# Optimization experiments

Hardware: AMD Instinct MI355X
Metric: run time of the kernel (lower is better)

The kernel has to match this reference:

```python
import jax, jax.numpy as jnp
import numpy as np

WS = 8          # window_size
SHIFT = 4       # shift_size
HEADS = 12
C = 384
HD = C // HEADS
SCALE = HD ** -0.5
N = WS * WS


def _rel_pos_index(Wh, Ww):
    # double_step_seq(2*Ww-1, Wh, 1, Ww) -> (1, Wh*Ww); idx = rel + rel.T; flip along axis 1
    seq1 = np.arange(0, (2 * Ww - 1) * Wh, 2 * Ww - 1)
    seq2 = np.arange(0, Ww)
    rel = (seq1[:, None] + seq2[None, :]).reshape(1, -1)
    idx = rel + rel.T
    return np.flip(idx, 1).copy()

REL_IDX = jnp.asarray(_rel_pos_index(WS, WS))  # [N, N] int


def window_partition(x, ws):
    # x: [B, H, W, C] -> [B*nW, ws*ws, C]
    B, H, W, Cc = x.shape
    x = x.reshape(B, H // ws, ws, W // ws, ws, Cc).transpose(0, 1, 3, 2, 4, 5)
    return x.reshape(-1, ws * ws, Cc)


def window_reverse(win, H, W, ws):
    B = win.shape[0] // ((H // ws) * (W // ws))
    x = win.reshape(B, H // ws, W // ws, ws, ws, -1).transpose(0, 1, 3, 2, 4, 5)
    return x.reshape(B, H, W, -1)


def _attn_mask(H, W, ws, shift):
    # region ids 0..8 per (h,w) as in the torch slice loop
    hi = np.arange(H)
    wi = np.arange(W)
    h_id = (hi >= H - ws).astype(np.int32) + (hi >= H - shift).astype(np.int32)
    w_id = (wi >= W - ws).astype(np.int32) + (wi >= W - shift).astype(np.int32)
    cnt = (h_id[:, None] * 3 + w_id[None, :]).astype(np.float32)
    img = jnp.asarray(cnt)[None, :, :, None]              # [1, H, W, 1]
    mw = window_partition(img, ws).reshape(-1, ws * ws)   # [nW, N]
    diff = mw[:, None, :] - mw[:, :, None]                # [nW, N, N]
    return jnp.where(diff != 0, jnp.float32(-100.0), jnp.float32(0.0))


def setup_inputs() -> dict:
    key = jax.random.key(0)
    ks = jax.random.split(key, 8)
    B, H, W = 16, 96, 96
    std = 0.02
    return {
        "query": jax.random.normal(ks[0], (B, H * W, C), jnp.float32),
        "skip_query": jax.random.normal(ks[1], (B, H * W, C), jnp.float32),
        "W_qkv": jax.random.normal(ks[2], (C, 2 * C), jnp.float32) * std,
        "b_qkv": jnp.zeros((2 * C,), jnp.float32),
        "W_skip": jax.random.normal(ks[3], (C, C), jnp.float32) * std,
        "b_skip": jnp.zeros((C,), jnp.float32),
        "rpb_table": jax.random.normal(ks[4], ((2 * WS - 1) * (2 * WS - 1), HEADS), jnp.float32) * std,
        "W_proj": jax.random.normal(ks[5], (C, C), jnp.float32) * std,
        "b_proj": jnp.zeros((C,), jnp.float32),
        "h": H,
        "w": W,
    }


def reference(query, skip_query, W_qkv, b_qkv, W_skip, b_skip, rpb_table, W_proj, b_proj, h, w):
    B, L, Cc = query.shape
    q4 = query.reshape(B, h, w, Cc)
    s4 = skip_query.reshape(B, h, w, Cc)
    pad_r = (WS - w % WS) % WS
    pad_b = (WS - h % WS) % WS
    q4 = jnp.pad(q4, ((0, 0), (0, pad_b), (0, pad_r), (0, 0)))
    s4 = jnp.pad(s4, ((0, 0), (0, pad_b), (0, pad_r), (0, 0)))
    H_pad, W_pad = q4.shape[1], q4.shape[2]

    # cyclic shift
    q4 = jnp.roll(q4, (-SHIFT, -SHIFT), axis=(1, 2))
    s4 = jnp.roll(s4, (-SHIFT, -SHIFT), axis=(1, 2))
    mask = _attn_mask(H_pad, W_pad, WS, SHIFT)  # [nW, N, N]

    xw = window_partition(q4, WS)   # [Bn, N, C] -> k, v source
    sw = window_partition(s4, WS)   # [Bn, N, C] -> q source
    Bn = xw.shape[0]

    kv = (xw @ W_qkv + b_qkv).reshape(Bn, N, 2, HEADS, HD)
    k = kv[:, :, 0].transpose(0, 2, 1, 3)   # [Bn, H, N, d]
    v = kv[:, :, 1].transpose(0, 2, 1, 3)
    q = ((sw @ W_skip + b_skip).reshape(Bn, N, HEADS, HD).transpose(0, 2, 1, 3)) * SCALE

    attn = jnp.einsum('bhnd,bhmd->bhnm', q, k)  # [Bn, H, N, N]
    rpb = rpb_table[REL_IDX.reshape(-1)].reshape(N, N, HEADS).transpose(2, 0, 1)
    attn = attn + rpb[None]
    nW = mask.shape[0]
    attn = (attn.reshape(B, nW, HEADS, N, N) + mask[None, :, None]).reshape(Bn, HEADS, N, N)
    attn = jax.nn.softmax(attn, axis=-1)

    out = jnp.einsum('bhnm,bhmd->bhnd', attn, v).transpose(0, 2, 1, 3).reshape(Bn, N, Cc)
    out = out @ W_proj + b_proj

    x4 = window_reverse(out.reshape(-1, WS, WS, Cc), H_pad, W_pad, WS)
    x4 = jnp.roll(x4, (SHIFT, SHIFT), axis=(1, 2))
    x4 = x4[:, :h, :w]
    return x4.reshape(B, h * w, Cc)
```

## Files before the change

### kernel.cpp

```cpp
#include <hip/hip_runtime.h>
#include <hip/hip_bf16.h>


typedef __attribute__((ext_vector_type(8))) short short8;
typedef __attribute__((ext_vector_type(4))) float floatx4;

#define MFMA16(a, b, c) __builtin_amdgcn_mfma_f32_16x16x32_bf16(a, b, c, 0, 0, 0)

__device__ __forceinline__ short f2bf(float f) {
    __hip_bfloat16 h = __float2bfloat16(f);
    return *reinterpret_cast<short*>(&h);
}

__device__ __forceinline__ unsigned cvt2bf(float lo, float hi) {
    unsigned r;
    asm("v_cvt_pk_bf16_f32 %0, %1, %2" : "=v"(r) : "v"(lo), "v"(hi));
    return r;
}

__device__ __forceinline__ void glds16(const void* g, void* l) {
    __builtin_amdgcn_global_load_lds(
        (const __attribute__((address_space(1))) void*)g,
        (__attribute__((address_space(3))) void*)l, 16, 0, 0);
}

__device__ __forceinline__ void lds_fence() {
    asm volatile("s_waitcnt lgkmcnt(0)" ::: "memory");
    __builtin_amdgcn_sched_barrier(0);
}


__global__ __launch_bounds__(256) void prep_wt(const float* __restrict__ Wqkv,
                                               const float* __restrict__ Wskip,
                                               short* __restrict__ Wt) {
    int tid = blockIdx.x * 256 + threadIdx.x;
    if (tid >= 384 * 144) return;
    int k = tid / 144;
    int n8 = (tid % 144) * 8;
#pragma unroll
    for (int e = 0; e < 8; e++) {
        int n = n8 + e;
        float v = (n < 768) ? Wqkv[k * 768 + n]
                            : Wskip[k * 384 + (n - 768)] * 0.17677669529663687f;
        Wt[(size_t)n * 384 + k] = f2bf(v);
    }
}

__global__ __launch_bounds__(256) void prep_wtp(const float* __restrict__ Wproj,
                                                short* __restrict__ WtP) {
    int tid = blockIdx.x * 256 + threadIdx.x;
    if (tid >= 384 * 48) return;
    int k = tid / 48;
    int n8 = (tid % 48) * 8;
#pragma unroll
    for (int e = 0; e < 8; e++) {
        int n = n8 + e;
        WtP[(size_t)n * 384 + k] = f2bf(Wproj[k * 384 + n]);
    }
}

__global__ __launch_bounds__(256) void prep_bias(const float* __restrict__ rpb,
                                                 float* __restrict__ bias64) {
    int tid = blockIdx.x * 256 + threadIdx.x;
    if (tid >= 49152) return;
    int h = tid >> 12;
    int rem = tid & 4095;
    int i = rem >> 6, kk = rem & 63;
    int j = 63 - kk;
    int ridx = 15 * (i >> 3) + (i & 7) + 15 * (j >> 3) + (j & 7);
    bias64[tid] = rpb[ridx * 12 + h];
}

__global__ __launch_bounds__(768, 1) void fused_win(
    const float* __restrict__ xq, const float* __restrict__ xs,
    const short* __restrict__ Wt, const short* __restrict__ WtP,
    const float* __restrict__ bqkv, const float* __restrict__ bskip,
    const float* __restrict__ bproj, const float* __restrict__ bias64,
    float* __restrict__ out) {
    __shared__ short smem[73728];

    const int win = blockIdx.x;
    const int tid = threadIdx.x, lane = tid & 63, wid = tid >> 6;
    const int l15 = lane & 15, g4 = lane >> 4;
    const int al7 = l15 & 7;
    const int brd = (g4 ^ ((l15 ^ (l15 >> 2)) & 3)) * 8;

    const int b_img = win / 144, wr = win % 144;
    const int wy = wr / 12, wx = wr % 12;

    const int gr = tid / 12, gj = tid - gr * 12;
    int gyy = wy * 8 + (gr >> 3) + 4; if (gyy >= 96) gyy -= 96;
    int gxx = wx * 8 + (gr & 7) + 4;  if (gxx >= 96) gxx -= 96;
    const size_t grow = ((size_t)b_img * 9216 + gyy * 96 + gxx) * 384;
    short* lrow = smem + gr * 384;
    const int gr7 = gr & 7;

    auto gatherA = [&](const float* src) {
        const float* rb = src + grow;
#pragma unroll
        for (int cc = 0; cc < 4; cc++) {
            int c = gj * 4 + cc;
            float4 f0 = *(const float4*)(rb + c * 8);
            float4 f1 = *(const float4*)(rb + c * 8 + 4);
            uint4 u;
            u.x = cvt2bf(f0.x, f0.y); u.y = cvt2bf(f0.z, f0.w);
            u.z = cvt2bf(f1.x, f1.y); u.w = cvt2bf(f1.z, f1.w);
            *(uint4*)(lrow + ((c ^ gr7) * 8)) = u;
        }
    };

    const int swst = ((lane >> 2) ^ (lane >> 4)) & 3;
    int bso[2];
#pragma unroll
    for (int j = 0; j < 2; j++)
        bso[j] = (j * 16 + (lane >> 2)) * 384 + (((lane & 3) ^ swst) * 8);
    short* wsc = smem + 24576 + wid * 4096;

    const short* sK = Wt + (size_t)(wid * 32) * 384;
    const short* sV = Wt + (size_t)(384 + wid * 32) * 384;
    const short* sQ = Wt + (size_t)(768 + wid * 32) * 384;
    const short* sP = WtP + (size_t)(wid * 32) * 384;

#pragma unroll
    for (int s = 0; s < 2; s++)
#pragma unroll
        for (int j = 0; j < 2; j++)
            glds16(sQ + bso[j] + s * 32, wsc + s * 1024 + j * 512);
    gatherA(xs);
    __syncthreads();

    floatx4 aq[2][4];
#pragma unroll
    for (int a = 0; a < 2; a++)
#pragma unroll
        for (int b = 0; b < 4; b++)
#pragma unroll
            for (int r = 0; r < 4; r++) aq[a][b][r] = 0.f;
#pragma unroll
    for (int kt = 0; kt < 12; ++kt) {
        if (kt == 11) asm volatile("s_waitcnt vmcnt(0)" ::: "memory");
        else          asm volatile("s_waitcnt vmcnt(2)" ::: "memory");
        const int choff = ((kt * 4 + g4) ^ al7) * 8;
        short* hb = wsc + (kt & 1) * 1024;
        short8 af[4], bq[2];
#pragma unroll
        for (int b = 0; b < 4; b++)
            af[b] = *(const short8*)(smem + (b * 16 + l15) * 384 + choff);
#pragma unroll
        for (int a = 0; a < 2; a++)
            bq[a] = *(const short8*)(hb + (a * 16 + l15) * 32 + brd);
        __builtin_amdgcn_sched_barrier(0);
        asm volatile("s_waitcnt lgkmcnt(0)" ::: "memory");
        if (kt < 10) {
            int ko = (kt + 2) * 32;
#pragma unroll
            for (int j = 0; j < 2; j++) glds16(sQ + bso[j] + ko, hb + j * 512);
        }
        __builtin_amdgcn_sched_barrier(0);
#pragma unroll
        for (int a = 0; a < 2; a++)
#pragma unroll
            for (int b = 0; b < 4; b++)
                aq[a][b] = MFMA16(bq[a], af[b], aq[a][b]);
    }

    const float scl = 0.17677669529663687f;
#pragma unroll
    for (int a = 0; a < 2; a++) {
        float4 bv = *(const float4*)(bskip + wid * 32 + a * 16 + g4 * 4);
#pragma unroll
        for (int b = 0; b < 4; b++) {
            uint2 pk;
            pk.x = cvt2bf(aq[a][b][0] + bv.x * scl, aq[a][b][1] + bv.y * scl);
            pk.y = cvt2bf(aq[a][b][2] + bv.z * scl, aq[a][b][3] + bv.w * scl);
            *(uint2*)(wsc + 1024 + (b * 16 + l15) * 32 + a * 16 + g4 * 4) = pk;
        }
    }
    short8 qf[4];
#pragma unroll
    for (int nj = 0; nj < 4; nj++)
        qf[nj] = *(const short8*)(wsc + 1024 + (nj * 16 + l15) * 32 + g4 * 8);
    lds_fence();

#pragma unroll
    for (int s = 0; s < 2; s++)
#pragma unroll
        for (int j = 0; j < 2; j++) {
            glds16(sK + bso[j] + s * 32, wsc + s * 2048 + j * 512);
            glds16(sV + bso[j] + s * 32, wsc + s * 2048 + 1024 + j * 512);
        }
    __syncthreads();
    gatherA(xq);
    __syncthreads();

    floatx4 ak[2][4], av[2][4];
#pragma unroll
    for (int a = 0; a < 2; a++)
#pragma unroll
        for (int b = 0; b < 4; b++)
#pragma unroll
            for (int r = 0; r < 4; r++) { ak[a][b][r] = 0.f; av[a][b][r] = 0.f; }
#pragma unroll
    for (int kt = 0; kt < 12; ++kt) {
        if (kt == 11) asm volatile("s_waitcnt vmcnt(0)" ::: "memory");
        else          asm volatile("s_waitcnt vmcnt(4)" ::: "memory");
        const int choff = ((kt * 4 + g4) ^ al7) * 8;
        short* hb = wsc + (kt & 1) * 2048;
        short8 af[4], bk[2], bv2[2];
#pragma unroll
        for (int b = 0; b < 4; b++)
            af[b] = *(const short8*)(smem + (b * 16 + l15) * 384 + choff);
#pragma unroll
        for (int a = 0; a < 2; a++) {
            bk[a]  = *(const short8*)(hb + (a * 16 + l15) * 32 + brd);
            bv2[a] = *(const short8*)(hb + 1024 + (a * 16 + l15) * 32 + brd);
        }
        __builtin_amdgcn_sched_barrier(0);
        asm volatile("s_waitcnt lgkmcnt(0)" ::: "memory");
        if (kt < 10) {
            int ko = (kt + 2) * 32;
#pragma unroll
            for (int j = 0; j < 2; j++) {
                glds16(sK + bso[j] + ko, hb + j * 512);
                glds16(sV + bso[j] + ko, hb + 1024 + j * 512);
            }
        }
        __builtin_amdgcn_sched_barrier(0);
#pragma unroll
        for (int a = 0; a < 2; a++)
#pragma unroll
            for (int b = 0; b < 4; b++) {
                ak[a][b] = MFMA16(bk[a], af[b], ak[a][b]);
                av[a][b] = MFMA16(af[b], bv2[a], av[a][b]);
            }
    }
    __syncthreads();

#pragma unroll
    for (int a = 0; a < 2; a++) {
        float4 bv = *(const float4*)(bqkv + wid * 32 + a * 16 + g4 * 4);
#pragma unroll
        for (int b = 0; b < 4; b++) {
            uint2 pk;
            pk.x = cvt2bf(ak[a][b][0] + bv.x, ak[a][b][1] + bv.y);
            pk.y = cvt2bf(ak[a][b][2] + bv.z, ak[a][b][3] + bv.w);
            *(uint2*)(wsc + (b * 16 + l15) * 32 + a * 16 + g4 * 4) = pk;
        }
    }
#pragma unroll
    for (int a = 0; a < 2; a++) {
        float bvs = bqkv[384 + wid * 32 + a * 16 + l15];
#pragma unroll
        for (int b = 0; b < 4; b++) {
            uint2 pk;
            pk.x = cvt2bf(av[a][b][0] + bvs, av[a][b][1] + bvs);
            pk.y = cvt2bf(av[a][b][2] + bvs, av[a][b][3] + bvs);
            int tch = b * 2 + (g4 >> 1);
            *(uint2*)(wsc + 2048 + (a * 16 + l15) * 64 +
                      ((tch ^ (l15 & 7)) * 8) + (g4 & 1) * 4) = pk;
        }
    }
    short8 kf[4], vf[2][2];
#pragma unroll
    for (int mi = 0; mi < 4; mi++)
        kf[mi] = *(const short8*)(wsc + (mi * 16 + l15) * 32 + g4 * 8);
#pragma unroll
    for (int ma = 0; ma < 2; ma++)
#pragma unroll
        for (int ks = 0; ks < 2; ks++)
            vf[ma][ks] = *(const short8*)(wsc + 2048 + (ma * 16 + l15) * 64 +
                                          (((ks * 4 + g4) ^ (l15 & 7)) * 8));

    floatx4 st[4][4];
#pragma unroll
    for (int mi = 0; mi < 4; mi++)
#pragma unroll
        for (int nj = 0; nj < 4; nj++)
#pragma unroll
            for (int r = 0; r < 4; r++) st[mi][nj][r] = 0.f;
#pragma unroll
    for (int mi = 0; mi < 4; mi++)
#pragma unroll
        for (int nj = 0; nj < 4; nj++)
            st[mi][nj] = MFMA16(kf[mi], qf[nj], st[mi][nj]);

    const float* bb = bias64 + wid * 4096;
#pragma unroll
    for (int nj = 0; nj < 4; nj++) {
        int i = nj * 16 + l15;
#pragma unroll
        for (int mi = 0; mi < 4; mi++) {
            floatx4 b4 = *(const floatx4*)(bb + i * 64 + mi * 16 + g4 * 4);
            st[mi][nj] += b4;
        }
    }

    if (wy == 11 || wx == 11) {
        int wy11 = (wy == 11), wx11 = (wx == 11);
        int ri[4];
#pragma unroll
        for (int nj = 0; nj < 4; nj++) {
            int t = nj * 16 + l15;
            int hh = wy11 ? (((t >> 3) >= 4) ? 2 : 1) : 0;
            int ww = wx11 ? (((t & 7) >= 4) ? 2 : 1) : 0;
            ri[nj] = hh * 3 + ww;
        }
#pragma unroll
        for (int mi = 0; mi < 4; mi++)
#pragma unroll
            for (int r = 0; r < 4; r++) {
                int t = mi * 16 + g4 * 4 + r;
                int hh = wy11 ? (((t >> 3) >= 4) ? 2 : 1) : 0;
                int ww = wx11 ? (((t & 7) >= 4) ? 2 : 1) : 0;
                int rk = hh * 3 + ww;
#pragma unroll
                for (int nj = 0; nj < 4; nj++)
                    if (rk != ri[nj]) st[mi][nj][r] -= 100.0f;
            }
    }

    float rden[4];
#pragma unroll
    for (int nj = 0; nj < 4; nj++) {
        float m = -1e30f;
#pragma unroll
        for (int mi = 0; mi < 4; mi++)
#pragma unroll
            for (int r = 0; r < 4; r++) m = fmaxf(m, st[mi][nj][r]);
        m = fmaxf(m, __shfl_xor(m, 16));
        m = fmaxf(m, __shfl_xor(m, 32));
        float s = 0.f;
#pragma unroll
        for (int mi = 0; mi < 4; mi++)
#pragma unroll
            for (int r = 0; r < 4; r++) {
                float p = __expf(st[mi][nj][r] - m);
                st[mi][nj][r] = p;
                s += p;
            }
        s += __shfl_xor(s, 16);
        s += __shfl_xor(s, 32);
        rden[nj] = 1.0f / s;
    }

#pragma unroll
    for (int mi = 0; mi < 4; mi++)
#pragma unroll
        for (int nj = 0; nj < 4; nj++) {
            uint2 pk;
            pk.x = cvt2bf(st[mi][nj][0], st[mi][nj][1]);
            pk.y = cvt2bf(st[mi][nj][2], st[mi][nj][3]);
            int kch = mi * 2 + (g4 >> 1);
            *(uint2*)(wsc + (nj * 16 + l15) * 64 +
                      ((kch ^ (l15 & 7)) * 8) + (g4 & 1) * 4) = pk;
        }

    floatx4 o[2][4];
#pragma unroll
    for (int ma = 0; ma < 2; ma++)
#pragma unroll
        for (int nj = 0; nj < 4; nj++)
#pragma unroll
            for (int r = 0; r < 4; r++) o[ma][nj][r] = 0.f;
#pragma unroll
    for (int ks = 0; ks < 2; ks++) {
        short8 pb[4];
#pragma unroll
        for (int nj = 0; nj < 4; nj++)
            pb[nj] = *(const short8*)(wsc + (nj * 16 + l15) * 64 +
                                      (((ks * 4 + g4) ^ (l15 & 7)) * 8));
#pragma unroll
        for (int ma = 0; ma < 2; ma++)
#pragma unroll
            for (int nj = 0; nj < 4; nj++)
                o[ma][nj] = MFMA16(vf[ma][ks], pb[nj], o[ma][nj]);
    }
    lds_fence();

#pragma unroll
    for (int s = 0; s < 2; s++)
#pragma unroll
        for (int j = 0; j < 2; j++)
            glds16(sP + bso[j] + s * 32, wsc + s * 1024 + j * 512);

#pragma unroll
    for (int ma = 0; ma < 2; ma++)
#pragma unroll
        for (int nj = 0; nj < 4; nj++) {
            int i = nj * 16 + l15;
            uint2 pk;
            pk.x = cvt2bf(o[ma][nj][0] * rden[nj], o[ma][nj][1] * rden[nj]);
            pk.y = cvt2bf(o[ma][nj][2] * rden[nj], o[ma][nj][3] * rden[nj]);
            int ch = wid * 4 + ma * 2 + (g4 >> 1);
            *(uint2*)(smem + i * 384 + ((ch ^ (i & 7)) * 8) + (g4 & 1) * 4) = pk;
        }
    __syncthreads();

    floatx4 ap[2][4];
#pragma unroll
    for (int a = 0; a < 2; a++)
#pragma unroll
        for (int b = 0; b < 4; b++)
#pragma unroll
            for (int r = 0; r < 4; r++) ap[a][b][r] = 0.f;
#pragma unroll
    for (int kt = 0; kt < 12; ++kt) {
        if (kt == 11) asm volatile("s_waitcnt vmcnt(0)" ::: "memory");
        else          asm volatile("s_waitcnt vmcnt(2)" ::: "memory");
        const int choff = ((kt * 4 + g4) ^ al7) * 8;
        short* hb = wsc + (kt & 1) * 1024;
        short8 af[4], bp[2];
#pragma unroll
        for (int b = 0; b < 4; b++)
            af[b] = *(const short8*)(smem + (b * 16 + l15) * 384 + choff);
#pragma unroll
        for (int a = 0; a < 2; a++)
            bp[a] = *(const short8*)(hb + (a * 16 + l15) * 32 + brd);
        __builtin_amdgcn_sched_barrier(0);
        asm volatile("s_waitcnt lgkmcnt(0)" ::: "memory");
        if (kt < 10) {
            int ko = (kt + 2) * 32;
#pragma unroll
            for (int j = 0; j < 2; j++) glds16(sP + bso[j] + ko, hb + j * 512);
        }
        __builtin_amdgcn_sched_barrier(0);
#pragma unroll
        for (int a = 0; a < 2; a++)
#pragma unroll
            for (int b = 0; b < 4; b++)
                ap[a][b] = MFMA16(bp[a], af[b], ap[a][b]);
    }

#pragma unroll
    for (int a = 0; a < 2; a++) {
        int n = wid * 32 + a * 16 + g4 * 4;
        float4 bv = *(const float4*)(bproj + n);
#pragma unroll
        for (int b = 0; b < 4; b++) {
            int t = b * 16 + l15;
            int yy = wy * 8 + (t >> 3) + 4; if (yy >= 96) yy -= 96;
            int xx = wx * 8 + (t & 7) + 4;  if (xx >= 96) xx -= 96;
            floatx4 ov = ap[a][b];
            ov[0] += bv.x; ov[1] += bv.y; ov[2] += bv.z; ov[3] += bv.w;
            *(floatx4*)(&out[((size_t)b_img * 9216 + yy * 96 + xx) * 384 + n]) = ov;
        }
    }
}

extern "C" void kernel_launch(void* const* d_in, const int* in_sizes, int n_in,
                              void* d_out, int out_size, void* d_ws, size_t ws_size,
                              hipStream_t stream) {
    const float* query = (const float*)d_in[0];
    const float* skipq = (const float*)d_in[1];
    const float* Wqkv  = (const float*)d_in[2];
    const float* bqkv  = (const float*)d_in[3];
    const float* Wskip = (const float*)d_in[4];
    const float* bskip = (const float*)d_in[5];
    const float* rpb   = (const float*)d_in[6];
    const float* Wproj = (const float*)d_in[7];
    const float* bproj = (const float*)d_in[8];
    float* out = (float*)d_out;

    int M = in_sizes[0] / 384;
    int nwin = M / 64;

    char* ws = (char*)d_ws;
    size_t off = 0;
    auto alloc = [&](size_t bytes) -> void* {
        void* p = ws + off;
        off = (off + bytes + 255) & ~(size_t)255;
        return p;
    };
    short* Wt     = (short*)alloc((size_t)1152 * 384 * 2);
    short* WtP    = (short*)alloc((size_t)384 * 384 * 2);
    float* bias64 = (float*)alloc((size_t)12 * 64 * 64 * 4);
    (void)ws_size;

    hipLaunchKernelGGL(prep_wt, dim3(216), dim3(256), 0, stream, Wqkv, Wskip, Wt);
    hipLaunchKernelGGL(prep_wtp, dim3(72), dim3(256), 0, stream, Wproj, WtP);
    hipLaunchKernelGGL(prep_bias, dim3(192), dim3(256), 0, stream, rpb, bias64);
    hipLaunchKernelGGL(fused_win, dim3(nwin), dim3(768), 0, stream,
                       query, skipq, Wt, WtP, bqkv, bskip, bproj, bias64, out);
}
```

Before: 498.5 us.

## Prefetch query rows into registers, swizzle Q/K LDS staging, coalesce output stores

The fp32 query rows for the K/V projection are now loaded into registers early, overlapping the Q-projection loop, and converted to bf16 into LDS afterwards instead of running a second gather. The Q and K LDS staging buffers get an XOR swizzle to reduce bank conflicts on their write/read patterns. The output epilogue goes through LDS with a swizzled layout so each wave writes contiguous 128-byte row segments instead of scattered 16-byte stores. In exchange it uses 32 more VGPRs for the prefetched rows, which may hurt occupancy, and adds an extra LDS round trip in the epilogue.

```diff
diff --git a/kernel.cpp b/kernel.cpp
--- a/kernel.cpp
+++ b/kernel.cpp
@@ -127,6 +127,15 @@
         for (int j = 0; j < 2; j++)
             glds16(sQ + bso[j] + s * 32, wsc + s * 1024 + j * 512);
     gatherA(xs);
+    float4 xr[8];
+    {
+        const float* rb = xq + grow;
+#pragma unroll
+        for (int cc = 0; cc < 4; cc++) {
+            xr[cc * 2]     = *(const float4*)(rb + (gj * 4 + cc) * 8);
+            xr[cc * 2 + 1] = *(const float4*)(rb + (gj * 4 + cc) * 8 + 4);
+        }
+    }
     __syncthreads();
 
     floatx4 aq[2][4];
@@ -173,13 +182,17 @@
             uint2 pk;
             pk.x = cvt2bf(aq[a][b][0] + bv.x * scl, aq[a][b][1] + bv.y * scl);
             pk.y = cvt2bf(aq[a][b][2] + bv.z * scl, aq[a][b][3] + bv.w * scl);
-            *(uint2*)(wsc + 1024 + (b * 16 + l15) * 32 + a * 16 + g4 * 4) = pk;
+            int row = b * 16 + l15;
+            int phys = (a * 2 + (g4 >> 1)) ^ (row & 3);
+            *(uint2*)(wsc + 1024 + row * 32 + phys * 8 + (g4 & 1) * 4) = pk;
         }
     }
     short8 qf[4];
 #pragma unroll
-    for (int nj = 0; nj < 4; nj++)
-        qf[nj] = *(const short8*)(wsc + 1024 + (nj * 16 + l15) * 32 + g4 * 8);
+    for (int nj = 0; nj < 4; nj++) {
+        int row = nj * 16 + l15;
+        qf[nj] = *(const short8*)(wsc + 1024 + row * 32 + ((g4 ^ (row & 3)) * 8));
+    }
     lds_fence();
 
 #pragma unroll
@@ -190,7 +203,16 @@
             glds16(sV + bso[j] + s * 32, wsc + s * 2048 + 1024 + j * 512);
         }
     __syncthreads();
-    gatherA(xq);
+#pragma unroll
+    for (int cc = 0; cc < 4; cc++) {
+        int c = gj * 4 + cc;
+        uint4 u;
+        u.x = cvt2bf(xr[cc * 2].x, xr[cc * 2].y);
+        u.y = cvt2bf(xr[cc * 2].z, xr[cc * 2].w);
+        u.z = cvt2bf(xr[cc * 2 + 1].x, xr[cc * 2 + 1].y);
+        u.w = cvt2bf(xr[cc * 2 + 1].z, xr[cc * 2 + 1].w);
+        *(uint4*)(lrow + ((c ^ gr7) * 8)) = u;
+    }
     __syncthreads();
 
     floatx4 ak[2][4], av[2][4];
@@ -244,7 +266,9 @@
             uint2 pk;
             pk.x = cvt2bf(ak[a][b][0] + bv.x, ak[a][b][1] + bv.y);
             pk.y = cvt2bf(ak[a][b][2] + bv.z, ak[a][b][3] + bv.w);
-            *(uint2*)(wsc + (b * 16 + l15) * 32 + a * 16 + g4 * 4) = pk;
+            int row = b * 16 + l15;
+            int phys = (a * 2 + (g4 >> 1)) ^ (row & 3);
+            *(uint2*)(wsc + row * 32 + phys * 8 + (g4 & 1) * 4) = pk;
         }
     }
 #pragma unroll
@@ -262,8 +286,10 @@
     }
     short8 kf[4], vf[2][2];
 #pragma unroll
-    for (int mi = 0; mi < 4; mi++)
-        kf[mi] = *(const short8*)(wsc + (mi * 16 + l15) * 32 + g4 * 8);
+    for (int mi = 0; mi < 4; mi++) {
+        int row = mi * 16 + l15;
+        kf[mi] = *(const short8*)(wsc + row * 32 + ((g4 ^ (row & 3)) * 8));
+    }
 #pragma unroll
     for (int ma = 0; ma < 2; ma++)
 #pragma unroll
@@ -431,18 +457,30 @@
                 ap[a][b] = MFMA16(bp[a], af[b], ap[a][b]);
     }
 
+    float* fsc = (float*)wsc;
 #pragma unroll
     for (int a = 0; a < 2; a++) {
-        int n = wid * 32 + a * 16 + g4 * 4;
-        float4 bv = *(const float4*)(bproj + n);
+        float4 bv = *(const float4*)(bproj + wid * 32 + a * 16 + g4 * 4);
 #pragma unroll
         for (int b = 0; b < 4; b++) {
-            int t = b * 16 + l15;
-            int yy = wy * 8 + (t >> 3) + 4; if (yy >= 96) yy -= 96;
-            int xx = wx * 8 + (t & 7) + 4;  if (xx >= 96) xx -= 96;
+            int row = b * 16 + l15;
+            int phys = (a * 4 + g4) ^ (row & 7);
             floatx4 ov = ap[a][b];
             ov[0] += bv.x; ov[1] += bv.y; ov[2] += bv.z; ov[3] += bv.w;
-            *(floatx4*)(&out[((size_t)b_img * 9216 + yy * 96 + xx) * 384 + n]) = ov;
+            *(floatx4*)(fsc + row * 32 + phys * 4) = ov;
+        }
+    }
+    lds_fence();
+    {
+        const int r8 = lane >> 3, c8 = lane & 7;
+#pragma unroll
+        for (int it = 0; it < 8; it++) {
+            int row = it * 8 + r8;
+            floatx4 ov = *(const floatx4*)(fsc + row * 32 + ((c8 ^ r8) * 4));
+            int yy = wy * 8 + (row >> 3) + 4; if (yy >= 96) yy -= 96;
+            int xx = wx * 8 + (row & 7) + 4;  if (xx >= 96) xx -= 96;
+            *(floatx4*)(&out[((size_t)b_img * 9216 + yy * 96 + xx) * 384 +
+                             wid * 32 + c8 * 4]) = ov;
         }
     }
 }
```

After: 464.7 us. 6.8% less time.
